# Performance work log

Hardware: AMD Instinct MI355X
Metric: run time of the kernel (lower is better)

The kernel has to match this reference:

```python
import jax, jax.numpy as jnp
import numpy as np

B, T, C = 16, 4096, 128
CODEBOOK_SIZE = 1024


def setup_inputs() -> dict:
    key = jax.random.key(0)
    kx, ke = jax.random.split(key)
    x = jax.random.normal(kx, (B, T, C), dtype=jnp.float32)
    embed = jax.random.normal(ke, (CODEBOOK_SIZE, C), dtype=jnp.float32)
    return {"x": x, "embed": embed}


def reference(x, embed):
    # x: [B, T, C], embed: [K, C]
    b, t, c = x.shape
    flat = x.reshape(b * t, c)                      # [BT, C]
    # distance = -||x - e||^2, expanded so we never materialize [BT, K, C]
    x_sq = jnp.sum(flat * flat, axis=-1, keepdims=True)   # [BT, 1]
    e_sq = jnp.sum(embed * embed, axis=-1)                 # [K]
    dist = 2.0 * (flat @ embed.T) - x_sq - e_sq[None, :]   # [BT, K]
    embed_ind = jnp.argmax(dist, axis=-1).reshape(b, t)    # [B, T]
    quantized = embed[embed_ind]                           # [B, T, C] gather
    return quantized, embed_ind
```

## Files before the change

### kernel.cpp

```cpp
#include <hip/hip_runtime.h>
#include <float.h>


#define Cdim        128
#define KCODES      1024
#define CH          64
#define NCH         16
#define BROWS       128
#define THREADS     256
#define FRAG_OFF    4096
#define CHUNK_BYTES 32768

typedef _Float16 f16;
typedef __attribute__((ext_vector_type(8)))  _Float16 f16x8;
typedef __attribute__((ext_vector_type(16))) float    f32x16;

__global__ __launch_bounds__(256) void esq_kernel(const float* __restrict__ embed,
                                                  float* __restrict__ esq, int K) {
    int gid  = blockIdx.x * blockDim.x + threadIdx.x;
    int code = gid >> 6;
    int lane = threadIdx.x & 63;
    if (code >= K) return;
    float2 v = ((const float2*)(embed + (size_t)code * Cdim))[lane];
    float  s = fmaf(v.x, v.x, v.y * v.y);
    #pragma unroll
    for (int m = 32; m >= 1; m >>= 1) s += __shfl_xor(s, m, 64);
    if (lane == 0) esq[code] = s;
}

__device__ __forceinline__ void cvt8(float4 a, float4 b, f16x8& h, f16x8& lo) {
    float v[8] = {a.x, a.y, a.z, a.w, b.x, b.y, b.z, b.w};
    #pragma unroll
    for (int i = 0; i < 8; ++i) {
        f16 hh = (f16)v[i];
        h[i]  = hh;
        lo[i] = (f16)(v[i] - (float)hh);
    }
}

__global__ __launch_bounds__(256) void bconv_kernel(const float* __restrict__ embed,
                                                    char* __restrict__ img) {
    int t    = blockIdx.x * 256 + threadIdx.x;
    int code = t >> 4;
    int seg  = t & 15;
    int kk   = seg >> 1;
    int lh   = seg & 1;
    const float4* p = (const float4*)(embed + (size_t)code * Cdim + kk * 16 + lh * 8);
    float4 v0 = p[0], v1 = p[1];
    f16x8 h, lo;
    cvt8(v0, v1, h, lo);
    int ch = code >> 6, n = (code >> 5) & 1, lm = code & 31;
    size_t base = FRAG_OFF + (size_t)ch * CHUNK_BYTES
                + (size_t)(((n * 8 + kk) * 2 + lh) * 512 + lm * 16);
    *(f16x8*)(img + base)         = h;
    *(f16x8*)(img + base + 16384) = lo;
}

__device__ __forceinline__ void gll16(const void* g, void* l) {
    __builtin_amdgcn_global_load_lds(
        (const __attribute__((address_space(1))) unsigned int*)g,
        (__attribute__((address_space(3))) unsigned int*)l, 16, 0, 0);
}

__global__ __launch_bounds__(THREADS, 2) void vq_kernel(
    const float* __restrict__ x, const float* __restrict__ embed,
    const char* __restrict__ ws, float* __restrict__ outq,
    float* __restrict__ outi) {

    __shared__ __align__(16) char  Bb[2][CHUNK_BYTES];
    __shared__ __align__(16) float esq_lds[KCODES];
    __shared__ int winners[BROWS];

    const int tid  = threadIdx.x;
    const int wid  = tid >> 6;
    const int l    = tid & 63;
    const int lm   = l & 31;
    const int lh   = l >> 5;
    const int row0 = blockIdx.x * BROWS;

    const char* frag = ws + FRAG_OFF;

    {
        const char* src = frag + wid * 8192 + (size_t)l * 16;
        char*       dst = &Bb[0][wid * 8192];
        #pragma unroll
        for (int i = 0; i < 8; ++i) gll16(src + i * 1024, dst + i * 1024);
        gll16(ws + wid * 1024 + (size_t)l * 16, (char*)esq_lds + wid * 1024);
    }

    f16x8 ah[8], al[8];
    {
        const float* xr = x + (size_t)(row0 + wid * 32 + lm) * Cdim + lh * 8;
        #pragma unroll
        for (int kk = 0; kk < 8; ++kk) {
            float4 v0 = *(const float4*)(xr + kk * 16);
            float4 v1 = *(const float4*)(xr + kk * 16 + 4);
            cvt8(v0, v1, ah[kk], al[kk]);
        }
    }

    float best[16]; int bidx[16];
    #pragma unroll
    for (int r = 0; r < 16; ++r) { best[r] = -FLT_MAX; bidx[r] = 0; }

    #pragma unroll 1
    for (int ch = 0; ch < NCH; ++ch) {
        const int cur = ch & 1, nxt = cur ^ 1;

        __builtin_amdgcn_s_barrier();

        if (ch + 1 < NCH) {
            const char* src = frag + (size_t)(ch + 1) * CHUNK_BYTES
                            + wid * 8192 + (size_t)l * 16;
            char* dst = &Bb[nxt][wid * 8192];
            #pragma unroll
            for (int i = 0; i < 8; ++i) gll16(src + i * 1024, dst + i * 1024);
            asm volatile("s_waitcnt vmcnt(8)" ::: "memory");
        } else {
            asm volatile("s_waitcnt vmcnt(0)" ::: "memory");
        }
        __builtin_amdgcn_s_barrier();

        const float eq0 = esq_lds[ch * CH + lm];
        const float eq1 = esq_lds[ch * CH + 32 + lm];

        f32x16 a00, a01, a10, a11, a20, a21;
        #pragma unroll
        for (int r = 0; r < 16; ++r) {
            a00[r] = 0.f; a01[r] = 0.f; a10[r] = 0.f;
            a11[r] = 0.f; a20[r] = 0.f; a21[r] = 0.f;
        }

        const char* bb = &Bb[cur][(size_t)l * 16];
        #pragma unroll
        for (int kk = 0; kk < 8; ++kk) {
            f16x8 bh0 = *(const f16x8*)(bb + kk * 1024);
            f16x8 bh1 = *(const f16x8*)(bb + 8192  + kk * 1024);
            f16x8 bl0 = *(const f16x8*)(bb + 16384 + kk * 1024);
            f16x8 bl1 = *(const f16x8*)(bb + 24576 + kk * 1024);
            a00 = __builtin_amdgcn_mfma_f32_32x32x16_f16(ah[kk], bh0, a00, 0, 0, 0);
            a01 = __builtin_amdgcn_mfma_f32_32x32x16_f16(ah[kk], bh1, a01, 0, 0, 0);
            a10 = __builtin_amdgcn_mfma_f32_32x32x16_f16(ah[kk], bl0, a10, 0, 0, 0);
            a11 = __builtin_amdgcn_mfma_f32_32x32x16_f16(ah[kk], bl1, a11, 0, 0, 0);
            a20 = __builtin_amdgcn_mfma_f32_32x32x16_f16(al[kk], bh0, a20, 0, 0, 0);
            a21 = __builtin_amdgcn_mfma_f32_32x32x16_f16(al[kk], bh1, a21, 0, 0, 0);
        }

        const int code0 = ch * CH + lm;
        #pragma unroll
        for (int r = 0; r < 16; ++r) {
            float s0 = fmaf(2.f, (a00[r] + a10[r]) + a20[r], -eq0);
            float s1 = fmaf(2.f, (a01[r] + a11[r]) + a21[r], -eq1);
            if (s0 > best[r]) { best[r] = s0; bidx[r] = code0; }
            if (s1 > best[r]) { best[r] = s1; bidx[r] = code0 + 32; }
        }
    }

    #pragma unroll
    for (int r = 0; r < 16; ++r) {
        float bs = best[r]; int bi = bidx[r];
        #pragma unroll
        for (int m = 1; m <= 16; m <<= 1) {
            float vs = __shfl_xor(bs, m, 64);
            int   vi = __shfl_xor(bi, m, 64);
            if (vs > bs || (vs == bs && vi < bi)) { bs = vs; bi = vi; }
        }
        if (lm == 0) {
            int grow = wid * 32 + (r & 3) + 8 * (r >> 2) + 4 * lh;
            winners[grow] = bi;
            outi[row0 + grow] = (float)bi;
        }
    }
    __syncthreads();

    #pragma unroll
    for (int i = 0; i < 16; ++i) {
        int pos = i * 256 + tid;
        int r = pos >> 5, c4 = pos & 31;
        int idx = winners[r];
        float4 v = ((const float4*)(embed + (size_t)idx * Cdim))[c4];
        ((float4*)(outq + (size_t)(row0 + r) * Cdim))[c4] = v;
    }
}

extern "C" void kernel_launch(void* const* d_in, const int* in_sizes, int n_in,
                              void* d_out, int out_size, void* d_ws, size_t ws_size,
                              hipStream_t stream) {
    const float* x     = (const float*)d_in[0];
    const float* embed = (const float*)d_in[1];
    const int M = in_sizes[0] / Cdim;
    const int K = in_sizes[1] / Cdim;
    float* outq = (float*)d_out;
    float* outi = outq + (size_t)M * Cdim;

    esq_kernel <<<K / 4, 256, 0, stream>>>(embed, (float*)d_ws, K);
    bconv_kernel<<<64,    256, 0, stream>>>(embed, (char*)d_ws);
    vq_kernel  <<<M / BROWS, THREADS, 0, stream>>>(x, embed, (const char*)d_ws,
                                                   outq, outi);
}
```

Measured before the change: 75.95 us.

## Double block to 8 waves, reduce accumulators, and interleave MFMA phases with barriers

Raises rows per block to 256 with 512 threads, so each wave loads half as much of each codebook chunk into LDS. The inner loop is split into four phases, each bracketed by barriers and s_setprio, with the next-chunk prefetch issued in the first phase. Accumulators drop from six to four by summing the hi and lo products into shared registers. The block cuts per-wave staging cost and tries to overlap loads with MFMA, at the price of more barriers, fewer blocks and a single-block occupancy risk from the launch bound.

```diff
diff --git a/kernel.cpp b/kernel.cpp
--- a/kernel.cpp
+++ b/kernel.cpp
@@ -6,8 +6,8 @@
 #define KCODES      1024
 #define CH          64
 #define NCH         16
-#define BROWS       128
-#define THREADS     256
+#define BROWS       256
+#define THREADS     512
 #define FRAG_OFF    4096
 #define CHUNK_BYTES 32768
 
@@ -81,11 +81,12 @@
     const char* frag = ws + FRAG_OFF;
 
     {
-        const char* src = frag + wid * 8192 + (size_t)l * 16;
-        char*       dst = &Bb[0][wid * 8192];
-        #pragma unroll
-        for (int i = 0; i < 8; ++i) gll16(src + i * 1024, dst + i * 1024);
-        gll16(ws + wid * 1024 + (size_t)l * 16, (char*)esq_lds + wid * 1024);
+        const char* src = frag + wid * 4096 + (size_t)l * 16;
+        char*       dst = &Bb[0][wid * 4096];
+        #pragma unroll
+        for (int i = 0; i < 4; ++i) gll16(src + i * 1024, dst + i * 1024);
+        if (wid < 4)
+            gll16(ws + wid * 1024 + (size_t)l * 16, (char*)esq_lds + wid * 1024);
     }
 
     f16x8 ah[8], al[8];
@@ -107,50 +108,60 @@
     for (int ch = 0; ch < NCH; ++ch) {
         const int cur = ch & 1, nxt = cur ^ 1;
 
-        __builtin_amdgcn_s_barrier();
-
-        if (ch + 1 < NCH) {
-            const char* src = frag + (size_t)(ch + 1) * CHUNK_BYTES
-                            + wid * 8192 + (size_t)l * 16;
-            char* dst = &Bb[nxt][wid * 8192];
-            #pragma unroll
-            for (int i = 0; i < 8; ++i) gll16(src + i * 1024, dst + i * 1024);
-            asm volatile("s_waitcnt vmcnt(8)" ::: "memory");
-        } else {
-            asm volatile("s_waitcnt vmcnt(0)" ::: "memory");
-        }
+        asm volatile("s_waitcnt vmcnt(0)" ::: "memory");
         __builtin_amdgcn_s_barrier();
 
         const float eq0 = esq_lds[ch * CH + lm];
         const float eq1 = esq_lds[ch * CH + 32 + lm];
 
-        f32x16 a00, a01, a10, a11, a20, a21;
+        f32x16 a0, a1, a2, a3;
+        #pragma unroll
+        for (int r = 0; r < 16; ++r) { a0[r] = 0.f; a1[r] = 0.f; a2[r] = 0.f; a3[r] = 0.f; }
+
+        const char* bb = &Bb[cur][(size_t)l * 16];
+
+        #pragma unroll
+        for (int p = 0; p < 4; ++p) {
+            if (p == 0 && ch + 1 < NCH) {
+                const char* src = frag + (size_t)(ch + 1) * CHUNK_BYTES
+                                + wid * 4096 + (size_t)l * 16;
+                char* dst = &Bb[nxt][wid * 4096];
+                #pragma unroll
+                for (int i = 0; i < 4; ++i) gll16(src + i * 1024, dst + i * 1024);
+            }
+            const int k0 = 2 * p, k1 = 2 * p + 1;
+            f16x8 bh0a = *(const f16x8*)(bb + k0 * 1024);
+            f16x8 bh1a = *(const f16x8*)(bb + 8192  + k0 * 1024);
+            f16x8 bl0a = *(const f16x8*)(bb + 16384 + k0 * 1024);
+            f16x8 bl1a = *(const f16x8*)(bb + 24576 + k0 * 1024);
+            f16x8 bh0b = *(const f16x8*)(bb + k1 * 1024);
+            f16x8 bh1b = *(const f16x8*)(bb + 8192  + k1 * 1024);
+            f16x8 bl0b = *(const f16x8*)(bb + 16384 + k1 * 1024);
+            f16x8 bl1b = *(const f16x8*)(bb + 24576 + k1 * 1024);
+
+            __builtin_amdgcn_s_barrier();
+            __builtin_amdgcn_s_setprio(1);
+            a0 = __builtin_amdgcn_mfma_f32_32x32x16_f16(ah[k0], bh0a, a0, 0, 0, 0);
+            a2 = __builtin_amdgcn_mfma_f32_32x32x16_f16(ah[k0], bh1a, a2, 0, 0, 0);
+            a1 = __builtin_amdgcn_mfma_f32_32x32x16_f16(ah[k0], bl0a, a1, 0, 0, 0);
+            a3 = __builtin_amdgcn_mfma_f32_32x32x16_f16(ah[k0], bl1a, a3, 0, 0, 0);
+            a0 = __builtin_amdgcn_mfma_f32_32x32x16_f16(al[k0], bh0a, a0, 0, 0, 0);
+            a2 = __builtin_amdgcn_mfma_f32_32x32x16_f16(al[k0], bh1a, a2, 0, 0, 0);
+            a1 = __builtin_amdgcn_mfma_f32_32x32x16_f16(ah[k1], bl0b, a1, 0, 0, 0);
+            a3 = __builtin_amdgcn_mfma_f32_32x32x16_f16(ah[k1], bl1b, a3, 0, 0, 0);
+            a0 = __builtin_amdgcn_mfma_f32_32x32x16_f16(ah[k1], bh0b, a0, 0, 0, 0);
+            a2 = __builtin_amdgcn_mfma_f32_32x32x16_f16(ah[k1], bh1b, a2, 0, 0, 0);
+            a0 = __builtin_amdgcn_mfma_f32_32x32x16_f16(al[k1], bh0b, a0, 0, 0, 0);
+            a2 = __builtin_amdgcn_mfma_f32_32x32x16_f16(al[k1], bh1b, a2, 0, 0, 0);
+            __builtin_amdgcn_s_setprio(0);
+            __builtin_amdgcn_s_barrier();
+        }
+
+        const int code0 = ch * CH + lm;
         #pragma unroll
         for (int r = 0; r < 16; ++r) {
-            a00[r] = 0.f; a01[r] = 0.f; a10[r] = 0.f;
-            a11[r] = 0.f; a20[r] = 0.f; a21[r] = 0.f;
-        }
-
-        const char* bb = &Bb[cur][(size_t)l * 16];
-        #pragma unroll
-        for (int kk = 0; kk < 8; ++kk) {
-            f16x8 bh0 = *(const f16x8*)(bb + kk * 1024);
-            f16x8 bh1 = *(const f16x8*)(bb + 8192  + kk * 1024);
-            f16x8 bl0 = *(const f16x8*)(bb + 16384 + kk * 1024);
-            f16x8 bl1 = *(const f16x8*)(bb + 24576 + kk * 1024);
-            a00 = __builtin_amdgcn_mfma_f32_32x32x16_f16(ah[kk], bh0, a00, 0, 0, 0);
-            a01 = __builtin_amdgcn_mfma_f32_32x32x16_f16(ah[kk], bh1, a01, 0, 0, 0);
-            a10 = __builtin_amdgcn_mfma_f32_32x32x16_f16(ah[kk], bl0, a10, 0, 0, 0);
-            a11 = __builtin_amdgcn_mfma_f32_32x32x16_f16(ah[kk], bl1, a11, 0, 0, 0);
-            a20 = __builtin_amdgcn_mfma_f32_32x32x16_f16(al[kk], bh0, a20, 0, 0, 0);
-            a21 = __builtin_amdgcn_mfma_f32_32x32x16_f16(al[kk], bh1, a21, 0, 0, 0);
-        }
-
-        const int code0 = ch * CH + lm;
-        #pragma unroll
-        for (int r = 0; r < 16; ++r) {
-            float s0 = fmaf(2.f, (a00[r] + a10[r]) + a20[r], -eq0);
-            float s1 = fmaf(2.f, (a01[r] + a11[r]) + a21[r], -eq1);
+            float s0 = fmaf(2.f, a0[r] + a1[r], -eq0);
+            float s1 = fmaf(2.f, a2[r] + a3[r], -eq1);
             if (s0 > best[r]) { best[r] = s0; bidx[r] = code0; }
             if (s1 > best[r]) { best[r] = s1; bidx[r] = code0 + 32; }
         }
@@ -175,7 +186,7 @@
 
     #pragma unroll
     for (int i = 0; i < 16; ++i) {
-        int pos = i * 256 + tid;
+        int pos = i * THREADS + tid;
         int r = pos >> 5, c4 = pos & 31;
         int idx = winners[r];
         float4 v = ((const float4*)(embed + (size_t)idx * Cdim))[c4];
```

Result: slower. 78.76 us (+3.7%).

## Fold code-norm bias into an extra MFMA and swap operand roles with larger blocks

Applied to the files above, without the earlier changes.

Folds the -||e||^2 term into the matrix product as an extra k-slice: the negative norm is split into hi/lo halves paired with a constant ones vector, and x is pre-scaled by 2 before the split-f16 conversion. This removes the per-element fmaf epilogue and the separate esq LDS table. The block grows to 256 rows and 512 threads, with waves split across two codebook halves and merged through LDS. The codebook tile becomes the A operand, argmax runs per lane over codes, and a single accumulator chain replaces six partials, with the next fragment loads prefetched inside the loop. The single accumulator lengthens the MFMA dependency chain, and occupancy changes from two blocks per CU to one larger block.

```diff
diff --git a/kernel.cpp b/kernel.cpp
--- a/kernel.cpp
+++ b/kernel.cpp
@@ -6,9 +6,10 @@
 #define KCODES      1024
 #define CH          64
 #define NCH         16
-#define BROWS       128
-#define THREADS     256
-#define FRAG_OFF    4096
+#define BROWS       256
+#define THREADS     512
+#define KK8_OFF     4096
+#define IMG_OFF     36864
 #define CHUNK_BYTES 32768
 
 typedef _Float16 f16;
@@ -28,32 +29,47 @@
     if (lane == 0) esq[code] = s;
 }
 
-__device__ __forceinline__ void cvt8(float4 a, float4 b, f16x8& h, f16x8& lo) {
+__device__ __forceinline__ void cvt8s(float4 a, float4 b, float scale,
+                                      f16x8& h, f16x8& lo) {
     float v[8] = {a.x, a.y, a.z, a.w, b.x, b.y, b.z, b.w};
     #pragma unroll
     for (int i = 0; i < 8; ++i) {
-        f16 hh = (f16)v[i];
+        float s = v[i] * scale;
+        f16 hh = (f16)s;
         h[i]  = hh;
-        lo[i] = (f16)(v[i] - (float)hh);
+        lo[i] = (f16)(s - (float)hh);
     }
 }
 
 __global__ __launch_bounds__(256) void bconv_kernel(const float* __restrict__ embed,
-                                                    char* __restrict__ img) {
+                                                    const float* __restrict__ esq,
+                                                    char* __restrict__ ws) {
     int t    = blockIdx.x * 256 + threadIdx.x;
-    int code = t >> 4;
-    int seg  = t & 15;
-    int kk   = seg >> 1;
-    int lh   = seg & 1;
-    const float4* p = (const float4*)(embed + (size_t)code * Cdim + kk * 16 + lh * 8);
-    float4 v0 = p[0], v1 = p[1];
-    f16x8 h, lo;
-    cvt8(v0, v1, h, lo);
-    int ch = code >> 6, n = (code >> 5) & 1, lm = code & 31;
-    size_t base = FRAG_OFF + (size_t)ch * CHUNK_BYTES
-                + (size_t)(((n * 8 + kk) * 2 + lh) * 512 + lm * 16);
-    *(f16x8*)(img + base)         = h;
-    *(f16x8*)(img + base + 16384) = lo;
+    int code = t / 18;
+    int slot = t % 18;
+    int kk   = slot >> 1;
+    int lh   = slot & 1;
+    int ch = code >> 6, nt = (code >> 5) & 1, lm = code & 31;
+    if (kk < 8) {
+        const float4* p = (const float4*)(embed + (size_t)code * Cdim + kk * 16 + lh * 8);
+        f16x8 h, lo;
+        cvt8s(p[0], p[1], 1.0f, h, lo);
+        size_t base = (size_t)IMG_OFF + (size_t)ch * CHUNK_BYTES + nt * 16384
+                    + kk * 1024 + lh * 512 + lm * 16;
+        *(f16x8*)(ws + base)        = h;
+        *(f16x8*)(ws + base + 8192) = lo;
+    } else {
+        f16x8 f = {};
+        if (lh == 0) {
+            float e2 = esq[code];
+            f16 e2h = (f16)e2;
+            f16 e2l = (f16)(e2 - (float)e2h);
+            f[0] = -e2h; f[1] = -e2l;
+        }
+        size_t base = (size_t)KK8_OFF + (size_t)ch * 2048 + nt * 1024
+                    + lh * 512 + lm * 16;
+        *(f16x8*)(ws + base) = f;
+    }
 }
 
 __device__ __forceinline__ void gll16(const void* g, void* l) {
@@ -62,120 +78,137 @@
         (__attribute__((address_space(3))) unsigned int*)l, 16, 0, 0);
 }
 
-__global__ __launch_bounds__(THREADS, 2) void vq_kernel(
+__global__ __launch_bounds__(THREADS) void vq_kernel(
     const float* __restrict__ x, const float* __restrict__ embed,
     const char* __restrict__ ws, float* __restrict__ outq,
     float* __restrict__ outi) {
 
     __shared__ __align__(16) char  Bb[2][CHUNK_BYTES];
-    __shared__ __align__(16) float esq_lds[KCODES];
-    __shared__ int winners[BROWS];
+    __shared__ __align__(16) char  Kk8[32768];
+    __shared__ float mrg_v[2][BROWS];
+    __shared__ int   mrg_i[2][BROWS];
+    __shared__ int   winners[BROWS];
 
     const int tid  = threadIdx.x;
     const int wid  = tid >> 6;
     const int l    = tid & 63;
     const int lm   = l & 31;
     const int lh   = l >> 5;
+    const int nt   = wid >> 2;
+    const int wr   = wid & 3;
     const int row0 = blockIdx.x * BROWS;
-
-    const char* frag = ws + FRAG_OFF;
+    const int loff = lh * 512 + lm * 16;
 
     {
-        const char* src = frag + wid * 8192 + (size_t)l * 16;
-        char*       dst = &Bb[0][wid * 8192];
-        #pragma unroll
-        for (int i = 0; i < 8; ++i) gll16(src + i * 1024, dst + i * 1024);
-        gll16(ws + wid * 1024 + (size_t)l * 16, (char*)esq_lds + wid * 1024);
-    }
-
-    f16x8 ah[8], al[8];
-    {
-        const float* xr = x + (size_t)(row0 + wid * 32 + lm) * Cdim + lh * 8;
+        const char* src0 = ws + IMG_OFF + wid * 4096 + (size_t)l * 16;
+        char*       dst0 = &Bb[0][wid * 4096];
+        #pragma unroll
+        for (int i = 0; i < 4; ++i) gll16(src0 + i * 1024, dst0 + i * 1024);
+        const char* src1 = ws + KK8_OFF + wid * 4096 + (size_t)l * 16;
+        char*       dst1 = Kk8 + wid * 4096;
+        #pragma unroll
+        for (int i = 0; i < 4; ++i) gll16(src1 + i * 1024, dst1 + i * 1024);
+    }
+
+    f16x8 bxh[2][8], bxl[2][8];
+    #pragma unroll
+    for (int n = 0; n < 2; ++n) {
+        const float* xr = x + (size_t)(row0 + wr * 64 + n * 32 + lm) * Cdim + lh * 8;
         #pragma unroll
         for (int kk = 0; kk < 8; ++kk) {
             float4 v0 = *(const float4*)(xr + kk * 16);
             float4 v1 = *(const float4*)(xr + kk * 16 + 4);
-            cvt8(v0, v1, ah[kk], al[kk]);
-        }
-    }
-
-    float best[16]; int bidx[16];
-    #pragma unroll
-    for (int r = 0; r < 16; ++r) { best[r] = -FLT_MAX; bidx[r] = 0; }
+            cvt8s(v0, v1, 2.0f, bxh[n][kk], bxl[n][kk]);
+        }
+    }
+
+    f16x8 bconst = {};
+    if (lh == 0) { bconst[0] = (f16)1.f; bconst[1] = (f16)1.f; }
+
+    float best0 = -FLT_MAX, best1 = -FLT_MAX;
+    int   bidx0 = 0,        bidx1 = 0;
+
+    asm volatile("s_waitcnt vmcnt(0)" ::: "memory");
+    __builtin_amdgcn_s_barrier();
 
     #pragma unroll 1
     for (int ch = 0; ch < NCH; ++ch) {
         const int cur = ch & 1, nxt = cur ^ 1;
 
         __builtin_amdgcn_s_barrier();
-
         if (ch + 1 < NCH) {
-            const char* src = frag + (size_t)(ch + 1) * CHUNK_BYTES
-                            + wid * 8192 + (size_t)l * 16;
-            char* dst = &Bb[nxt][wid * 8192];
+            const char* src = ws + IMG_OFF + (size_t)(ch + 1) * CHUNK_BYTES
+                            + wid * 4096 + (size_t)l * 16;
+            char* dst = &Bb[nxt][wid * 4096];
             #pragma unroll
-            for (int i = 0; i < 8; ++i) gll16(src + i * 1024, dst + i * 1024);
-            asm volatile("s_waitcnt vmcnt(8)" ::: "memory");
+            for (int i = 0; i < 4; ++i) gll16(src + i * 1024, dst + i * 1024);
+            asm volatile("s_waitcnt vmcnt(4)" ::: "memory");
         } else {
             asm volatile("s_waitcnt vmcnt(0)" ::: "memory");
         }
         __builtin_amdgcn_s_barrier();
 
-        const float eq0 = esq_lds[ch * CH + lm];
-        const float eq1 = esq_lds[ch * CH + 32 + lm];
-
-        f32x16 a00, a01, a10, a11, a20, a21;
+        f32x16 acc0, acc1;
+        #pragma unroll
+        for (int r = 0; r < 16; ++r) { acc0[r] = 0.f; acc1[r] = 0.f; }
+
+        const char* bbA = &Bb[cur][nt * 16384 + loff];
+        f16x8 ae8 = *(const f16x8*)(&Kk8[ch * 2048 + nt * 1024 + loff]);
+        f16x8 aeh = *(const f16x8*)(bbA);
+        f16x8 ael = *(const f16x8*)(bbA + 8192);
+
+        #pragma unroll
+        for (int kk = 0; kk < 8; ++kk) {
+            f16x8 aehN, aelN;
+            if (kk < 7) {
+                aehN = *(const f16x8*)(bbA + (kk + 1) * 1024);
+                aelN = *(const f16x8*)(bbA + 8192 + (kk + 1) * 1024);
+            }
+            acc0 = __builtin_amdgcn_mfma_f32_32x32x16_f16(aeh, bxh[0][kk], acc0, 0, 0, 0);
+            acc1 = __builtin_amdgcn_mfma_f32_32x32x16_f16(aeh, bxh[1][kk], acc1, 0, 0, 0);
+            acc0 = __builtin_amdgcn_mfma_f32_32x32x16_f16(ael, bxh[0][kk], acc0, 0, 0, 0);
+            acc1 = __builtin_amdgcn_mfma_f32_32x32x16_f16(ael, bxh[1][kk], acc1, 0, 0, 0);
+            acc0 = __builtin_amdgcn_mfma_f32_32x32x16_f16(aeh, bxl[0][kk], acc0, 0, 0, 0);
+            acc1 = __builtin_amdgcn_mfma_f32_32x32x16_f16(aeh, bxl[1][kk], acc1, 0, 0, 0);
+            aeh = aehN; ael = aelN;
+        }
+        acc0 = __builtin_amdgcn_mfma_f32_32x32x16_f16(ae8, bconst, acc0, 0, 0, 0);
+        acc1 = __builtin_amdgcn_mfma_f32_32x32x16_f16(ae8, bconst, acc1, 0, 0, 0);
+
+        const int cb = ch * CH + nt * 32 + lh * 4;
         #pragma unroll
         for (int r = 0; r < 16; ++r) {
-            a00[r] = 0.f; a01[r] = 0.f; a10[r] = 0.f;
-            a11[r] = 0.f; a20[r] = 0.f; a21[r] = 0.f;
-        }
-
-        const char* bb = &Bb[cur][(size_t)l * 16];
-        #pragma unroll
-        for (int kk = 0; kk < 8; ++kk) {
-            f16x8 bh0 = *(const f16x8*)(bb + kk * 1024);
-            f16x8 bh1 = *(const f16x8*)(bb + 8192  + kk * 1024);
-            f16x8 bl0 = *(const f16x8*)(bb + 16384 + kk * 1024);
-            f16x8 bl1 = *(const f16x8*)(bb + 24576 + kk * 1024);
-            a00 = __builtin_amdgcn_mfma_f32_32x32x16_f16(ah[kk], bh0, a00, 0, 0, 0);
-            a01 = __builtin_amdgcn_mfma_f32_32x32x16_f16(ah[kk], bh1, a01, 0, 0, 0);
-            a10 = __builtin_amdgcn_mfma_f32_32x32x16_f16(ah[kk], bl0, a10, 0, 0, 0);
-            a11 = __builtin_amdgcn_mfma_f32_32x32x16_f16(ah[kk], bl1, a11, 0, 0, 0);
-            a20 = __builtin_amdgcn_mfma_f32_32x32x16_f16(al[kk], bh0, a20, 0, 0, 0);
-            a21 = __builtin_amdgcn_mfma_f32_32x32x16_f16(al[kk], bh1, a21, 0, 0, 0);
-        }
-
-        const int code0 = ch * CH + lm;
-        #pragma unroll
-        for (int r = 0; r < 16; ++r) {
-            float s0 = fmaf(2.f, (a00[r] + a10[r]) + a20[r], -eq0);
-            float s1 = fmaf(2.f, (a01[r] + a11[r]) + a21[r], -eq1);
-            if (s0 > best[r]) { best[r] = s0; bidx[r] = code0; }
-            if (s1 > best[r]) { best[r] = s1; bidx[r] = code0 + 32; }
-        }
-    }
-
-    #pragma unroll
-    for (int r = 0; r < 16; ++r) {
-        float bs = best[r]; int bi = bidx[r];
-        #pragma unroll
-        for (int m = 1; m <= 16; m <<= 1) {
-            float vs = __shfl_xor(bs, m, 64);
-            int   vi = __shfl_xor(bi, m, 64);
-            if (vs > bs || (vs == bs && vi < bi)) { bs = vs; bi = vi; }
-        }
-        if (lm == 0) {
-            int grow = wid * 32 + (r & 3) + 8 * (r >> 2) + 4 * lh;
-            winners[grow] = bi;
-            outi[row0 + grow] = (float)bi;
-        }
+            const int code = cb + (r & 3) + 8 * (r >> 2);
+            float s0 = acc0[r], s1 = acc1[r];
+            if (s0 > best0) { best0 = s0; bidx0 = code; }
+            if (s1 > best1) { best1 = s1; bidx1 = code; }
+        }
+    }
+
+    {
+        float v; int vi;
+        v = __shfl_xor(best0, 32, 64); vi = __shfl_xor(bidx0, 32, 64);
+        if (v > best0 || (v == best0 && vi < bidx0)) { best0 = v; bidx0 = vi; }
+        v = __shfl_xor(best1, 32, 64); vi = __shfl_xor(bidx1, 32, 64);
+        if (v > best1 || (v == best1 && vi < bidx1)) { best1 = v; bidx1 = vi; }
+    }
+    if (lh == 0) {
+        mrg_v[nt][wr * 64 + lm]      = best0;  mrg_i[nt][wr * 64 + lm]      = bidx0;
+        mrg_v[nt][wr * 64 + 32 + lm] = best1;  mrg_i[nt][wr * 64 + 32 + lm] = bidx1;
     }
     __syncthreads();
+    if (tid < BROWS) {
+        float v0 = mrg_v[0][tid]; int i0 = mrg_i[0][tid];
+        float v1 = mrg_v[1][tid]; int i1 = mrg_i[1][tid];
+        int bi = (v1 > v0 || (v1 == v0 && i1 < i0)) ? i1 : i0;
+        winners[tid] = bi;
+        outi[row0 + tid] = (float)bi;
+    }
+    __syncthreads();
 
     #pragma unroll
     for (int i = 0; i < 16; ++i) {
-        int pos = i * 256 + tid;
+        int pos = i * THREADS + tid;
         int r = pos >> 5, c4 = pos & 31;
         int idx = winners[r];
         float4 v = ((const float4*)(embed + (size_t)idx * Cdim))[c4];
@@ -194,7 +227,7 @@
     float* outi = outq + (size_t)M * Cdim;
 
     esq_kernel <<<K / 4, 256, 0, stream>>>(embed, (float*)d_ws, K);
-    bconv_kernel<<<64,    256, 0, stream>>>(embed, (char*)d_ws);
+    bconv_kernel<<<72, 256, 0, stream>>>(embed, (const float*)d_ws, (char*)d_ws);
     vq_kernel  <<<M / BROWS, THREADS, 0, stream>>>(x, embed, (const char*)d_ws,
                                                    outq, outi);
 }
```

Result: faster. 68.81 us (-9.4%).
